# Kernel optimization log

Hardware: AMD Instinct MI355X
Metric: run time of the kernel (lower is better)

The kernel has to match this reference:

```python
import jax, jax.numpy as jnp
import numpy as np

B, N, DEG = 8, 8192, 16
E = B * N * DEG
K1 = 2458  # ceil(0.3*8192)
K2 = 738   # ceil(0.3*2458)
NUM_CLASSES = 10


def gat(x, src, dst, emask, W, a_s, a_d, bias):
    # PyG GATConv with add_self_loops=True, negative_slope=0.2, concat heads
    n = x.shape[0]
    H, F = a_s.shape
    xp = (x @ W).reshape(n, H, F)                      # [n,H,F]
    al_s = (xp * a_s).sum(-1)                          # [n,H]
    al_d = (xp * a_d).sum(-1)
    loops = jnp.arange(n, dtype=src.dtype)
    s2 = jnp.concatenate([src, loops])
    d2 = jnp.concatenate([dst, loops])
    m2 = jnp.concatenate([emask, jnp.ones(n, bool)])
    e = jax.nn.leaky_relu(al_s[s2] + al_d[d2], 0.2)    # [E+n,H]
    e = jnp.where(m2[:, None], e, -1e9)
    emax = jax.ops.segment_max(e, d2, num_segments=n)
    ex = jnp.where(m2[:, None], jnp.exp(e - emax[d2]), 0.0)
    den = jax.ops.segment_sum(ex, d2, num_segments=n)
    msg = ex[:, :, None] * xp[s2]                      # [E+n,H,F]
    out = jax.ops.segment_sum(msg, d2, num_segments=n) / den[:, :, None]
    return out.reshape(n, H * F) + bias


def inorm(x):
    # PyG InstanceNorm (affine=False): per-graph per-channel normalization
    xb = x.reshape(B, -1, x.shape[-1])
    mu = xb.mean(1, keepdims=True)
    var = ((xb - mu) ** 2).mean(1, keepdims=True)
    return ((xb - mu) / jnp.sqrt(var + 1e-5)).reshape(x.shape)


def topk_pool(x, src, dst, emask, p, k):
    # TopKPooling: score = tanh(x.p/|p|), keep top-k per graph, scale x by score
    n_tot = x.shape[0]
    n = n_tot // B
    score = jnp.tanh((x @ p) / jnp.linalg.norm(p))
    sv, si = jax.lax.top_k(score.reshape(B, n), k)     # [B,k]
    xg = jnp.take_along_axis(x.reshape(B, n, -1), si[:, :, None], axis=1)
    xnew = (xg * sv[:, :, None]).reshape(B * k, -1)
    perm = (si + (jnp.arange(B) * n)[:, None]).reshape(-1)
    newid = jnp.full(n_tot, -1, dtype=src.dtype).at[perm].set(
        jnp.arange(B * k, dtype=src.dtype))
    ns, nd = newid[src], newid[dst]
    m = emask & (ns >= 0) & (nd >= 0)
    return xnew, jnp.maximum(ns, 0), jnp.maximum(nd, 0), m


def setup_inputs() -> dict:
    key = jax.random.key(0)
    ks = jax.random.split(key, 32)
    pos = jax.random.normal(ks[0], (B * N, 3), jnp.float32)
    offs = jnp.repeat(jnp.arange(B, dtype=jnp.int32) * N, N * DEG)
    src = jax.random.randint(ks[1], (E,), 0, N, jnp.int32) + offs
    dst = jax.random.randint(ks[2], (E,), 0, N, jnp.int32) + offs

    def lin(k, fi, fo):
        return jax.random.normal(k, (fi, fo), jnp.float32) * (1.0 / np.sqrt(fi))

    d = dict(pos=pos, src=src, dst=dst)
    d['W1'] = lin(ks[3], 3, 32);   d['a_s1'] = jax.random.normal(ks[4], (2, 16)) * 0.2
    d['a_d1'] = jax.random.normal(ks[5], (2, 16)) * 0.2
    d['b1'] = jnp.zeros((32,));    d['p1'] = jax.random.normal(ks[6], (32,))
    d['W2'] = lin(ks[7], 32, 128); d['a_s2'] = jax.random.normal(ks[8], (2, 64)) * 0.2
    d['a_d2'] = jax.random.normal(ks[9], (2, 64)) * 0.2
    d['b2'] = jnp.zeros((128,));   d['p2'] = jax.random.normal(ks[10], (128,))
    d['W3'] = lin(ks[11], 128, 256); d['a_s3'] = jax.random.normal(ks[12], (1, 256)) * 0.1
    d['a_d3'] = jax.random.normal(ks[13], (1, 256)) * 0.1
    d['b3'] = jnp.zeros((256,))
    d['gw1'] = lin(ks[14], 256, 64);  d['gb1'] = jnp.zeros((64,))
    d['gw2'] = lin(ks[15], 64, 1);    d['gb2'] = jnp.zeros((1,))
    d['aw'] = lin(ks[16], 256, 256);  d['ab'] = jnp.zeros((256,))
    d['w1'] = lin(ks[17], 256, 512);  d['bb1'] = jnp.zeros((512,))
    d['w2'] = lin(ks[18], 512, 128);  d['bb2'] = jnp.zeros((128,))
    d['w3'] = lin(ks[19], 128, NUM_CLASSES); d['bb3'] = jnp.zeros((NUM_CLASSES,))
    return d


def reference(pos, src, dst, W1, a_s1, a_d1, b1, p1, W2, a_s2, a_d2, b2, p2,
              W3, a_s3, a_d3, b3, gw1, gb1, gw2, gb2, aw, ab,
              w1, bb1, w2, bb2, w3, bb3):
    emask = jnp.ones(src.shape[0], bool)
    x = gat(pos, src, dst, emask, W1, a_s1, a_d1, b1)
    x = jax.nn.elu(inorm(x))
    x, src, dst, emask = topk_pool(x, src, dst, emask, p1, K1)
    x = gat(x, src, dst, emask, W2, a_s2, a_d2, b2)
    x = jax.nn.elu(inorm(x))
    x, src, dst, emask = topk_pool(x, src, dst, emask, p2, K2)
    x = gat(x, src, dst, emask, W3, a_s3, a_d3, b3)
    x = jax.nn.elu(inorm(x))
    # GlobalAttention: gate_nn = Linear(256,64)+ELU+Linear(64,1); nn = Linear+ELU
    gate = jax.nn.elu(x @ gw1 + gb1) @ gw2 + gb2       # [M,1]
    h = jax.nn.elu(x @ aw + ab)                        # [M,256]
    a = jax.nn.softmax(gate.reshape(B, K2, 1), axis=1)
    g = (a * h.reshape(B, K2, 256)).sum(1)             # [B,256]
    z = jax.nn.elu(g @ w1 + bb1)   # dropout inactive in eval
    z = jax.nn.elu(z @ w2 + bb2)
    z = z @ w3 + bb3
    return jax.nn.log_softmax(z, axis=1)
```

## Files before the change

### kernel.cpp

```cpp
#include <hip/hip_runtime.h>
#include <cstdint>
#include <cstddef>

#define DI __device__ __forceinline__

namespace pk {

constexpr int NB1 = 65536;
constexpr int NE  = 1048576;
constexpr int BG  = 8;
constexpr int NPG1 = 8192;
constexpr int EPG1 = NE/BG;
constexpr int KP1 = 2458;
constexpr int KP2 = 738;
constexpr int NN2 = BG*KP1;
constexpr int NN3 = BG*KP2;
constexpr int REG2 = 16384;
constexpr int REG3 = 4096;
constexpr int CAP2 = BG*REG2;
constexpr int CAP3 = BG*REG3;

DI float lrelu(float x){ return x > 0.f ? x : 0.2f*x; }
DI float eluf(float x){ return x > 0.f ? x : expf(x) - 1.f; }

DI int swz_block(){
  int nb = gridDim.x, b = blockIdx.x;
  if((nb & 7) == 0) return (b & 7)*(nb >> 3) + (b >> 3);
  return b;
}

__global__ __launch_bounds__(256) void k_xp1(
    const float* __restrict__ pos, const float* __restrict__ W,
    const float* __restrict__ as_, const float* __restrict__ ad_,
    float* __restrict__ xp, float* __restrict__ als, float* __restrict__ ald){
  int i = blockIdx.x*256 + threadIdx.x;
  if(i >= NB1) return;
  float p0=pos[3*i], p1=pos[3*i+1], p2=pos[3*i+2];
  float row[32];
#pragma unroll
  for(int c=0;c<32;c++) row[c] = p0*W[c] + p1*W[32+c] + p2*W[64+c];
  float s0=0.f,d0=0.f,s1=0.f,d1=0.f;
#pragma unroll
  for(int f=0;f<16;f++){
    s0 += row[f]*as_[f];        d0 += row[f]*ad_[f];
    s1 += row[16+f]*as_[16+f];  d1 += row[16+f]*ad_[16+f];
  }
  float4* o = reinterpret_cast<float4*>(xp + (size_t)i*32);
#pragma unroll
  for(int q=0;q<8;q++) o[q] = make_float4(row[4*q],row[4*q+1],row[4*q+2],row[4*q+3]);
  als[2*i]=s0; als[2*i+1]=s1; ald[2*i]=d0; ald[2*i+1]=d1;
}

__global__ __launch_bounds__(1024) void k_tile_count(
    const int* __restrict__ de, int* __restrict__ cnt){
  __shared__ int h[256];
  int tid = threadIdx.x;
  int g = blockIdx.x & 7, t = blockIdx.x >> 3;
  int lo = g*NPG1 + t*256;
  if(tid < 256) h[tid] = 0;
  __syncthreads();
  const int4* de4 = (const int4*)(de + g*EPG1);
  for(int it=0; it<4; it++){
    int4 buf[8];
#pragma unroll
    for(int j=0;j<8;j++) buf[j] = de4[(it*8+j)*1024 + tid];
#pragma unroll
    for(int j=0;j<8;j++){
      int4 b = buf[j];
      int d0=b.x-lo, d1=b.y-lo, d2=b.z-lo, d3=b.w-lo;
      if((unsigned)d0<256u) atomicAdd(&h[d0],1);
      if((unsigned)d1<256u) atomicAdd(&h[d1],1);
      if((unsigned)d2<256u) atomicAdd(&h[d2],1);
      if((unsigned)d3<256u) atomicAdd(&h[d3],1);
    }
  }
  __syncthreads();
  if(tid < 256) cnt[lo + tid] = h[tid];
}

__global__ __launch_bounds__(1024) void k_tile_scatter(
    const int* __restrict__ se, const int* __restrict__ de,
    const int* __restrict__ rowptr, int* __restrict__ eo){
  __shared__ int cur[256];
  int tid = threadIdx.x;
  int g = blockIdx.x & 7, t = blockIdx.x >> 3;
  int lo = g*NPG1 + t*256;
  if(tid < 256) cur[tid] = rowptr[lo + tid];
  __syncthreads();
  const int4* de4 = (const int4*)(de + g*EPG1);
  const int4* se4 = (const int4*)(se + g*EPG1);
  for(int it=0; it<4; it++){
    int4 bd[8], bs[8];
#pragma unroll
    for(int j=0;j<8;j++){
      int idx = (it*8+j)*1024 + tid;
      bd[j] = de4[idx]; bs[j] = se4[idx];
    }
#pragma unroll
    for(int j=0;j<8;j++){
      int4 d = bd[j], s = bs[j];
      int d0=d.x-lo; if((unsigned)d0<256u){ int p=atomicAdd(&cur[d0],1); eo[p]=s.x; }
      int d1=d.y-lo; if((unsigned)d1<256u){ int p=atomicAdd(&cur[d1],1); eo[p]=s.y; }
      int d2=d.z-lo; if((unsigned)d2<256u){ int p=atomicAdd(&cur[d2],1); eo[p]=s.z; }
      int d3=d.w-lo; if((unsigned)d3<256u){ int p=atomicAdd(&cur[d3],1); eo[p]=s.w; }
    }
  }
}

__global__ __launch_bounds__(256) void k_scatter_r(
    const int* __restrict__ se, const int* __restrict__ de,
    const int* __restrict__ gcnt, int reg,
    int* __restrict__ cursor, int* __restrict__ eo){
  int i = swz_block()*256 + threadIdx.x;
  int g = i / reg, loc = i % reg;
  if(loc < gcnt[g]){
    int p = atomicAdd(&cursor[de[i]], 1);
    eo[p] = se[i];
  }
}

__global__ __launch_bounds__(256) void k_edge_compact(
    const int* __restrict__ se, const int* __restrict__ de,
    const int* __restrict__ gcnt_in, int fixed_in, int bpg, int reg_in,
    const int* __restrict__ newid, int* __restrict__ gcnt_out,
    int* __restrict__ ons, int* __restrict__ ond, int reg_out,
    int* __restrict__ cnt){
  __shared__ int s_a[4096];
  __shared__ int s_b[4096];
  __shared__ int run, tbase;
  int tid = threadIdx.x;
  if(tid == 0) run = 0;
  __syncthreads();
  int blk = swz_block();
  int g = blk / bpg, t = blk % bpg;
  int mg = gcnt_in ? gcnt_in[g] : fixed_in;
  if(mg > reg_in) mg = reg_in;
  int base_l = t*4096;
  if(base_l < mg){
    const int* deb = de + (size_t)g*reg_in + base_l;
    const int* seb = se + (size_t)g*reg_in + base_l;
    const int4* de4 = (const int4*)deb;
    const int4* se4 = (const int4*)seb;
    int4 BD[4], BS[4];
#pragma unroll
    for(int j=0;j<4;j++){ BD[j]=de4[j*256+tid]; BS[j]=se4[j*256+tid]; }
#pragma unroll
    for(int j=0;j<4;j++){
      int eb = base_l + (j*256+tid)*4;
      int dd[4]={BD[j].x,BD[j].y,BD[j].z,BD[j].w};
      int ss[4]={BS[j].x,BS[j].y,BS[j].z,BS[j].w};
#pragma unroll
      for(int q=0;q<4;q++){
        if(eb+q < mg){
          int a = newid[ss[q]], b = newid[dd[q]];
          if(a>=0 && b>=0){
            int p = atomicAdd(&run, 1);
            s_a[p]=a; s_b[p]=b;
            atomicAdd(&cnt[b], 1);
          }
        }
      }
    }
  }
  __syncthreads();
  int ns = run;
  if(tid==0) tbase = ns ? atomicAdd(&gcnt_out[g], ns) : 0;
  __syncthreads();
  int tb = tbase;
  for(int j=tid; j<ns; j+=256){
    int s2 = tb + j;
    if(s2 < reg_out){ ons[(size_t)g*reg_out+s2]=s_a[j]; ond[(size_t)g*reg_out+s2]=s_b[j]; }
  }
}

__global__ __launch_bounds__(1024) void k_scan_g(
    const int* __restrict__ cnt, int R, int estride,
    int* __restrict__ rowptr, int* __restrict__ cursor){
  __shared__ int wsum[16];
  int g = blockIdx.x;
  int tid = threadIdx.x, lane = tid & 63, w = tid >> 6;
  int PER = (R + 1023) >> 10;
  int base = g*R;
  int i0 = tid*PER;
  int v[8]; int s = 0;
  for(int j=0;j<PER;j++){ int i=i0+j; int x=(i<R)?cnt[base+i]:0; v[j]=s; s+=x; }
  int inc = s;
  for(int o=1;o<64;o<<=1){ int t=__shfl_up(inc,o,64); if(lane>=o) inc+=t; }
  if(lane==63) wsum[w]=inc;
  __syncthreads();
  int wb=0;
  for(int k=0;k<w;k++) wb+=wsum[k];
  int tb = g*estride + wb + inc - s;
  for(int j=0;j<PER;j++){
    int i=i0+j;
    if(i<R){
      int e=tb+v[j];
      rowptr[base+i]=e;
      if(cursor) cursor[base+i]=e;
    }
  }
}

template<int H,int F,int EB>
__global__ __launch_bounds__(256) void k_gat_fused(
    const float* __restrict__ xp, const float* __restrict__ als,
    const float* __restrict__ ald, const int* __restrict__ rowptr,
    const int* __restrict__ cnt, const int* __restrict__ esrc,
    const float* __restrict__ bias, float* __restrict__ out,
    float* __restrict__ accum, int RPG, int n){
  constexpr int C = H*F, C4 = C/4;
  constexpr int NPB = 256/C4;
  __shared__ float psum[4][C], psq[4][C];
  int tid = threadIdx.x;
  int nl = tid / C4, p = tid % C4;
  int node0 = swz_block()*NPB;
  int node = node0 + nl;
  int hh = (4*p)/F;
  const float4* xp4 = (const float4*)xp;
  float4 r = make_float4(0.f,0.f,0.f,0.f);
  bool valid = node < n;
  if(valid){
    float dvh = ald[node*H+hh];
    float sw  = expf(lrelu(als[node*H+hh] + dvh));
    float4 xs = xp4[(size_t)node*C4 + p];
    float den = sw;
    float ax=sw*xs.x, ay=sw*xs.y, az=sw*xs.z, aw_=sw*xs.w;
    int r0  = rowptr[node];
    int deg = cnt[node];
    for(int j=0; j<deg; j+=EB){
      int idx[EB]; float wv[EB]; float4 v[EB];
#pragma unroll
      for(int q=0;q<EB;q++)
        idx[q] = (j+q < deg) ? esrc[r0+j+q] : node;
#pragma unroll
      for(int q=0;q<EB;q++)
        wv[q] = als[idx[q]*H+hh];
#pragma unroll
      for(int q=0;q<EB;q++)
        v[q] = xp4[(size_t)idx[q]*C4 + p];
#pragma unroll
      for(int q=0;q<EB;q++){
        float w = (j+q < deg) ? expf(lrelu(wv[q] + dvh)) : 0.f;
        den += w;
        ax += w*v[q].x; ay += w*v[q].y; az += w*v[q].z; aw_ += w*v[q].w;
      }
    }
    float inv = 1.f / den;
    float4 bv = ((const float4*)bias)[p];
    r.x=ax*inv+bv.x; r.y=ay*inv+bv.y; r.z=az*inv+bv.z; r.w=aw_*inv+bv.w;
    ((float4*)out)[(size_t)node*C4 + p] = r;
  }
  int g0 = node0 / RPG;
  bool straddle = ((node0 + NPB - 1) / RPG) != g0;
  if(straddle){
    if(valid){
      int g = node / RPG;
      atomicAdd(&accum[(g*C+4*p+0)*2], r.x); atomicAdd(&accum[(g*C+4*p+0)*2+1], r.x*r.x);
      atomicAdd(&accum[(g*C+4*p+1)*2], r.y); atomicAdd(&accum[(g*C+4*p+1)*2+1], r.y*r.y);
      atomicAdd(&accum[(g*C+4*p+2)*2], r.z); atomicAdd(&accum[(g*C+4*p+2)*2+1], r.z*r.z);
      atomicAdd(&accum[(g*C+4*p+3)*2], r.w); atomicAdd(&accum[(g*C+4*p+3)*2+1], r.w*r.w);
    }
  } else {
    float sx=r.x, sy=r.y, sz=r.z, sw2=r.w;
    float qx=r.x*r.x, qy=r.y*r.y, qz=r.z*r.z, qw=r.w*r.w;
#pragma unroll
    for(int off=C4; off<64; off<<=1){
      sx += __shfl_down(sx, off, 64); sy += __shfl_down(sy, off, 64);
      sz += __shfl_down(sz, off, 64); sw2 += __shfl_down(sw2, off, 64);
      qx += __shfl_down(qx, off, 64); qy += __shfl_down(qy, off, 64);
      qz += __shfl_down(qz, off, 64); qw += __shfl_down(qw, off, 64);
    }
    int lane = tid & 63, w = tid >> 6;
    if(lane < C4){
      psum[w][4*lane+0]=sx; psum[w][4*lane+1]=sy;
      psum[w][4*lane+2]=sz; psum[w][4*lane+3]=sw2;
      psq[w][4*lane+0]=qx;  psq[w][4*lane+1]=qy;
      psq[w][4*lane+2]=qz;  psq[w][4*lane+3]=qw;
    }
    __syncthreads();
    if(tid < C){
      float ts = psum[0][tid]+psum[1][tid]+psum[2][tid]+psum[3][tid];
      float tq = psq[0][tid]+psq[1][tid]+psq[2][tid]+psq[3][tid];
      atomicAdd(&accum[(g0*C+tid)*2],   ts);
      atomicAdd(&accum[(g0*C+tid)*2+1], tq);
    }
  }
}

template<int K,int CO,int NPG,int H>
__global__ __launch_bounds__(256) void k_gemm_al(
    const float* __restrict__ X, const int* __restrict__ oldid,
    const float* __restrict__ scale, const float* __restrict__ W,
    float* __restrict__ Y, const float* __restrict__ a_s,
    const float* __restrict__ a_d, float* __restrict__ als,
    float* __restrict__ ald, int n){
  constexpr int SUB = 256/CO;
  constexpr int NB = SUB*NPG;
  __shared__ float xs[NB][K];
  __shared__ float ps[4][NPG], pd[4][NPG];
  int tid = threadIdx.x;
  int c = tid % CO, sg = tid / CO;
  int n0 = blockIdx.x * NB;
  for(int idx=tid; idx<NB*K; idx+=256){
    int r = idx / K, k = idx % K;
    int row = n0 + r;
    float v = 0.f;
    if(row < n){
      int orow = oldid[row];
      v = X[(size_t)orow*K + k] * scale[row];
    }
    xs[r][k] = v;
  }
  __syncthreads();
  float acc[NPG];
#pragma unroll
  for(int q=0;q<NPG;q++) acc[q]=0.f;
  for(int k=0;k<K;k++){
    float wv = W[(size_t)k*CO + c];
#pragma unroll
    for(int q=0;q<NPG;q++) acc[q] += xs[sg*NPG+q][k]*wv;
  }
  float asc = a_s[c], adc = a_d[c];
  float vs[NPG], vd[NPG];
#pragma unroll
  for(int q=0;q<NPG;q++){
    int row = n0 + sg*NPG + q;
    if(row < n) Y[(size_t)row*CO + c] = acc[q];
    vs[q] = acc[q]*asc; vd[q] = acc[q]*adc;
  }
#pragma unroll
  for(int o=32;o>0;o>>=1){
#pragma unroll
    for(int q=0;q<NPG;q++){
      vs[q] += __shfl_down(vs[q], o, 64);
      vd[q] += __shfl_down(vd[q], o, 64);
    }
  }
  int lane = tid & 63, w = tid >> 6;
  if(H == 2){
    if(lane == 0){
      int sg_ = w >> 1, h = w & 1;
#pragma unroll
      for(int q=0;q<NPG;q++){
        int row = n0 + sg_*NPG + q;
        if(row < n){ als[row*2+h] = vs[q]; ald[row*2+h] = vd[q]; }
      }
    }
  } else {
    if(lane == 0){
#pragma unroll
      for(int q=0;q<NPG;q++){ ps[w][q]=vs[q]; pd[w][q]=vd[q]; }
    }
    __syncthreads();
    if(tid < NPG){
      float s=0.f, d=0.f;
      for(int ww=0;ww<4;ww++){ s+=ps[ww][tid]; d+=pd[ww][tid]; }
      int row = n0 + tid;
      if(row < n){ als[row]=s; ald[row]=d; }
    }
  }
}

DI float inorm_of(const float* accum, int gc, float R, float x){
  float s = accum[gc*2], sq = accum[gc*2+1];
  float mu = s / R;
  float var = fmaxf(sq/R - mu*mu, 0.f);
  return eluf((x-mu)*rsqrtf(var+1e-5f));
}

template<int C>
__global__ __launch_bounds__(256) void k_inorm_score(
    float* __restrict__ x, const float* __restrict__ accum,
    const float* __restrict__ p, int R, int total,
    float* __restrict__ score, unsigned* __restrict__ u){
  __shared__ float rvp[256], rpp[256];
  int tid = threadIdx.x;
  int i = blockIdx.x*256 + tid;
  int c = tid & (C-1);
  bool act = i < total;
  float v = 0.f, pv = 0.f;
  if(act){
    int g = i / (R*C);
    v = inorm_of(accum, g*C+c, (float)R, x[i]);
    x[i] = v;
    pv = p[c];
  }
  rvp[tid] = v*pv; rpp[tid] = pv*pv;
  __syncthreads();
#pragma unroll
  for(int s2=C/2; s2>0; s2>>=1){
    if(c < s2){ rvp[tid]+=rvp[tid+s2]; rpp[tid]+=rpp[tid+s2]; }
    __syncthreads();
  }
  if(act && c==0){
    float sv = tanhf(rvp[tid]*rsqrtf(rpp[tid]));
    int row = i / C;
    score[row] = sv;
    unsigned bts = __float_as_uint(sv);
    u[row] = (bts & 0x80000000u) ? ~bts : (bts | 0x80000000u);
  }
}

__global__ __launch_bounds__(1024) void k_topk(
    const unsigned* __restrict__ u, const float* __restrict__ score,
    int R, int Ksel, int* __restrict__ newid, int* __restrict__ oldid,
    float* __restrict__ scale){
  __shared__ int hist[2048];
  __shared__ int seg[32];
  __shared__ int sh_b, sh_k;
  __shared__ int wsA[16], wsB[16];
  __shared__ int carr0, carr1;
  int g = blockIdx.x, tid = threadIdx.x, lane = tid&63, w = tid>>6;
  const unsigned* ug = u + (size_t)g*R;
  unsigned prefix = 0;
  int K = Ksel;
  for(int lev=0; lev<3; lev++){
    int shf = (lev==0)?21:((lev==1)?10:0);
    int nb  = (lev==2)?1024:2048;
    for(int i=tid;i<2048;i+=1024) hist[i]=0;
    __syncthreads();
    for(int i=tid;i<R;i+=1024){
      unsigned v = ug[i];
      bool ok = (lev==0) || (lev==1 && (v>>21)==prefix) || (lev==2 && (v>>10)==prefix);
      if(ok) atomicAdd(&hist[(v>>shf)&(nb-1)], 1);
    }
    __syncthreads();
    int W = nb/32;
    if(tid<32){ int s=0; int lo=nb-W*(tid+1); for(int b=lo;b<lo+W;b++) s+=hist[b]; seg[tid]=s; }
    __syncthreads();
    if(tid==0){
      int kk=K, sgi=0;
      while(seg[sgi]<kk){ kk-=seg[sgi]; sgi++; }
      int b = nb-1-W*sgi;
      while(hist[b]<kk){ kk-=hist[b]; b--; }
      sh_b=b; sh_k=kk;
    }
    __syncthreads();
    int b = sh_b; K = sh_k;
    if(lev==0) prefix = (unsigned)b;
    else if(lev==1) prefix = (prefix<<11) | (unsigned)b;
    else prefix = (prefix<<10) | (unsigned)b;
    __syncthreads();
  }
  unsigned thr = prefix;
  int need = K;
  if(tid==0){ carr0=0; carr1=0; }
  __syncthreads();
  for(int bb=0; bb<R; bb+=1024){
    int i = bb + tid; bool in = i < R;
    unsigned uv = in ? ug[i] : 0u;
    int eq = (in && uv==thr) ? 1:0;
    int gt = (in && uv>thr) ? 1:0;
    int inc = eq;
    for(int o=1;o<64;o<<=1){ int t=__shfl_up(inc,o,64); if(lane>=o) inc+=t; }
    if(lane==63) wsA[w]=inc;
    __syncthreads();
    int wb=0; for(int k=0;k<w;k++) wb+=wsA[k];
    int eq_excl = carr0 + wb + inc - eq;
    int take = (gt || (eq && eq_excl<need)) ? 1 : 0;
    int inc2 = take;
    for(int o=1;o<64;o<<=1){ int t=__shfl_up(inc2,o,64); if(lane>=o) inc2+=t; }
    if(lane==63) wsB[w]=inc2;
    __syncthreads();
    int wb2=0; for(int k=0;k<w;k++) wb2+=wsB[k];
    int pos = carr1 + wb2 + inc2 - take;
    if(take){
      int nr = g*Ksel + pos;
      newid[(size_t)g*R+i] = nr;
      oldid[nr] = g*R+i;
      scale[nr] = score[(size_t)g*R+i];
    }
    __syncthreads();
    if(tid==1023){ carr0 += wb + inc; carr1 += wb2 + inc2; }
    __syncthreads();
  }
}

__global__ __launch_bounds__(256) void k_gate_fused(
    const float* __restrict__ X, const float* __restrict__ accum,
    const float* __restrict__ gw1, const float* __restrict__ gb1,
    const float* __restrict__ gw2, const float* __restrict__ gb2,
    float* __restrict__ gatev, int n){
  __shared__ float xs[4][256];
  int tid = threadIdx.x;
  int n0 = blockIdx.x*4;
  for(int idx=tid; idx<1024; idx+=256){
    int r = idx >> 8, k = idx & 255;
    int row = n0 + r;
    float v = 0.f;
    if(row < n){
      int g = row / KP2;
      v = inorm_of(accum, g*256+k, (float)KP2, X[(size_t)row*256 + k]);
    }
    xs[r][k] = v;
  }
  __syncthreads();
  int sg = tid >> 6, c = tid & 63;
  float a = 0.f;
#pragma unroll 8
  for(int k=0;k<256;k++) a = fmaf(xs[sg][k], gw1[k*64+c], a);
  a = eluf(a + gb1[c]);
  float v = a * gw2[c];
#pragma unroll
  for(int o=32;o>0;o>>=1) v += __shfl_down(v, o, 64);
  if(c==0){
    int row = n0 + sg;
    if(row < n) gatev[row] = v + gb2[0];
  }
}

__global__ __launch_bounds__(256) void k_attn_gemm(
    const float* __restrict__ X, const float* __restrict__ accum,
    const float* __restrict__ W, const float* __restrict__ bias,
    const float* __restrict__ gatev, float* __restrict__ gvec){
  __shared__ float xs[4][256];
  __shared__ float red[256];
  int tid = threadIdx.x;
  int t = blockIdx.x, g = blockIdx.y;
  int r0 = t*4;
  float mx = -1e30f;
  for(int r=tid;r<KP2;r+=256) mx = fmaxf(mx, gatev[g*KP2+r]);
  red[tid]=mx; __syncthreads();
  for(int s=128;s>0;s>>=1){ if(tid<s) red[tid]=fmaxf(red[tid],red[tid+s]); __syncthreads(); }
  mx = red[0]; __syncthreads();
  float sm=0.f;
  for(int r=tid;r<KP2;r+=256) sm += expf(gatev[g*KP2+r]-mx);
  red[tid]=sm; __syncthreads();
  for(int s=128;s>0;s>>=1){ if(tid<s) red[tid]+=red[tid+s]; __syncthreads(); }
  float inv = 1.f/red[0];
  __syncthreads();
  for(int idx=tid; idx<1024; idx+=256){
    int r = idx >> 8, k = idx & 255;
    int lr = r0 + r;
    float v = 0.f;
    if(lr < KP2){
      int row = g*KP2 + lr;
      v = inorm_of(accum, g*256+k, (float)KP2, X[(size_t)row*256 + k]);
    }
    xs[r][k] = v;
  }
  __syncthreads();
  int c = tid;
  float acc[4];
#pragma unroll
  for(int q=0;q<4;q++) acc[q]=0.f;
  for(int k=0;k<256;k++){
    float wv = W[(size_t)k*256 + c];
#pragma unroll
    for(int q=0;q<4;q++) acc[q] += xs[q][k]*wv;
  }
  float bv = bias[c];
  float tot = 0.f;
#pragma unroll
  for(int q=0;q<4;q++){
    int lr = r0 + q;
    if(lr < KP2){
      float h = eluf(acc[q] + bv);
      tot += expf(gatev[g*KP2+lr]-mx) * h;
    }
  }
  atomicAdd(&gvec[g*256+c], tot*inv);
}

template<int K,int CO,int ACT>
__global__ __launch_bounds__(256) void k_mlp_t(
    const float* __restrict__ X, const float* __restrict__ W,
    const float* __restrict__ b, float* __restrict__ Y, int n){
  int i = blockIdx.x*256+threadIdx.x;
  if(i>=n*CO) return;
  int r=i/CO, c=i%CO;
  const float* xr = X + (size_t)r*K;
  float a=0.f;
#pragma unroll 16
  for(int k=0;k<K;k++) a = fmaf(xr[k], W[(size_t)k*CO+c], a);
  a += b[c];
  if(ACT) a = eluf(a);
  Y[i]=a;
}

__global__ __launch_bounds__(64) void k_head(
    const float* __restrict__ z2, const float* __restrict__ w3,
    const float* __restrict__ b3, float* __restrict__ out){
  __shared__ float zc[10]; __shared__ float mred, sred;
  int g=blockIdx.x, tid=threadIdx.x;
  if(tid<10){
    float a=0.f;
#pragma unroll 16
    for(int k=0;k<128;k++) a += z2[g*128+k]*w3[k*10+tid];
    zc[tid]=a+b3[tid];
  }
  __syncthreads();
  if(tid==0){
    float m=zc[0];
    for(int k=1;k<10;k++) m=fmaxf(m,zc[k]);
    float s=0.f;
    for(int k=0;k<10;k++) s+=expf(zc[k]-m);
    mred=m; sred=logf(s);
  }
  __syncthreads();
  if(tid<10) out[g*10+tid]=zc[tid]-mred-sred;
}

}

extern "C" void kernel_launch(void* const* d_in, const int* in_sizes, int n_in,
                              void* d_out, int out_size, void* d_ws, size_t ws_size,
                              hipStream_t stream){
  using namespace pk;
  (void)in_sizes; (void)n_in; (void)out_size;
  const float* pos = (const float*)d_in[0];
  const int*   src = (const int*)d_in[1];
  const int*   dst = (const int*)d_in[2];
  const float* W1  = (const float*)d_in[3];
  const float* as1 = (const float*)d_in[4];
  const float* ad1 = (const float*)d_in[5];
  const float* b1  = (const float*)d_in[6];
  const float* p1  = (const float*)d_in[7];
  const float* W2  = (const float*)d_in[8];
  const float* as2 = (const float*)d_in[9];
  const float* ad2 = (const float*)d_in[10];
  const float* b2  = (const float*)d_in[11];
  const float* p2  = (const float*)d_in[12];
  const float* W3  = (const float*)d_in[13];
  const float* as3 = (const float*)d_in[14];
  const float* ad3 = (const float*)d_in[15];
  const float* b3  = (const float*)d_in[16];
  const float* gw1 = (const float*)d_in[17];
  const float* gb1 = (const float*)d_in[18];
  const float* gw2 = (const float*)d_in[19];
  const float* gb2 = (const float*)d_in[20];
  const float* aw  = (const float*)d_in[21];
  const float* ab  = (const float*)d_in[22];
  const float* w1  = (const float*)d_in[23];
  const float* bb1 = (const float*)d_in[24];
  const float* w2  = (const float*)d_in[25];
  const float* bb2 = (const float*)d_in[26];
  const float* w3  = (const float*)d_in[27];
  const float* bb3 = (const float*)d_in[28];
  float* out = (float*)d_out;

  char* base = (char*)d_ws; size_t off = 0;
  auto alloc = [&](size_t nbytes)->char*{
    char* p = base + off; off = (off + nbytes + 255) & ~(size_t)255; return p;
  };
  int*   cnt2  = (int*)alloc((size_t)NN2*4);
  int*   cnt3  = (int*)alloc((size_t)NN3*4);
  int*   ecnt2 = (int*)alloc((size_t)BG*4);
  int*   ecnt3 = (int*)alloc((size_t)BG*4);
  float* acc1  = (float*)alloc((size_t)BG*32*2*4);
  float* acc2  = (float*)alloc((size_t)BG*128*2*4);
  float* acc3  = (float*)alloc((size_t)BG*256*2*4);
  float* gvec  = (float*)alloc((size_t)BG*256*4);
  size_t zend = off;
  int*   newid1 = (int*)alloc((size_t)NB1*4);
  int*   newid2 = (int*)alloc((size_t)NN2*4);
  size_t fstart = (size_t)((char*)newid1 - base);
  size_t fend = off;
  int*      cnt1   = (int*)alloc((size_t)NB1*4);
  float*    xp1    = (float*)alloc((size_t)NB1*32*4);
  float*    als1   = (float*)alloc((size_t)NB1*2*4);
  float*    ald1   = (float*)alloc((size_t)NB1*2*4);
  int*      rowptr1= (int*)alloc((size_t)NB1*4);
  int*      esrc1  = (int*)alloc((size_t)NE*4);
  float*    out1   = (float*)alloc((size_t)NB1*32*4);
  float*    score1 = (float*)alloc((size_t)NB1*4);
  unsigned* u1     = (unsigned*)alloc((size_t)NB1*4);
  int*      oldid1 = (int*)alloc((size_t)NN2*4);
  float*    scale1 = (float*)alloc((size_t)NN2*4);
  int*      ns2    = (int*)alloc((size_t)CAP2*4);
  int*      nd2    = (int*)alloc((size_t)CAP2*4);
  int*      rowptr2= (int*)alloc((size_t)NN2*4);
  int*      cursor2= (int*)alloc((size_t)NN2*4);
  int*      esrc2  = (int*)alloc((size_t)CAP2*4);
  float*    xp2    = (float*)alloc((size_t)NN2*128*4);
  float*    als2   = (float*)alloc((size_t)NN2*2*4);
  float*    ald2   = (float*)alloc((size_t)NN2*2*4);
  float*    out2   = (float*)alloc((size_t)NN2*128*4);
  float*    score2 = (float*)alloc((size_t)NN2*4);
  unsigned* u2     = (unsigned*)alloc((size_t)NN2*4);
  int*      oldid2 = (int*)alloc((size_t)NN3*4);
  float*    scale2 = (float*)alloc((size_t)NN3*4);
  int*      ns3    = (int*)alloc((size_t)CAP3*4);
  int*      nd3    = (int*)alloc((size_t)CAP3*4);
  int*      rowptr3= (int*)alloc((size_t)NN3*4);
  int*      cursor3= (int*)alloc((size_t)NN3*4);
  int*      esrc3  = (int*)alloc((size_t)CAP3*4);
  float*    xp3    = (float*)alloc((size_t)NN3*256*4);
  float*    als3   = (float*)alloc((size_t)NN3*4);
  float*    ald3   = (float*)alloc((size_t)NN3*4);
  float*    out3   = (float*)alloc((size_t)NN3*256*4);
  float*    gatev  = (float*)alloc((size_t)NN3*4);
  float*    z1     = (float*)alloc((size_t)BG*512*4);
  float*    z2     = (float*)alloc((size_t)BG*128*4);
  if(off > ws_size) return;

  auto cdiv = [](int a, int b){ return (a+b-1)/b; };

  hipMemsetAsync(base, 0, zend, stream);
  hipMemsetAsync(base + fstart, 0xFF, fend - fstart, stream);

  k_xp1<<<cdiv(NB1,256),256,0,stream>>>(pos,W1,as1,ad1,xp1,als1,ald1);
  k_tile_count<<<256,1024,0,stream>>>(dst,cnt1);
  k_scan_g<<<BG,1024,0,stream>>>(cnt1,NPG1,EPG1,rowptr1,nullptr);
  k_tile_scatter<<<256,1024,0,stream>>>(src,dst,rowptr1,esrc1);
  k_gat_fused<2,16,8><<<NB1/32,256,0,stream>>>(xp1,als1,ald1,rowptr1,cnt1,esrc1,b1,out1,acc1,NPG1,NB1);
  k_inorm_score<32><<<cdiv(NB1*32,256),256,0,stream>>>(out1,acc1,p1,8192,NB1*32,score1,u1);
  k_topk<<<BG,1024,0,stream>>>(u1,score1,8192,KP1,newid1,oldid1,scale1);
  k_edge_compact<<<BG*32,256,0,stream>>>(src,dst,nullptr,EPG1,32,EPG1,newid1,ecnt2,ns2,nd2,REG2,cnt2);
  k_scan_g<<<BG,1024,0,stream>>>(cnt2,KP1,REG2,rowptr2,cursor2);
  k_scatter_r<<<CAP2/256,256,0,stream>>>(ns2,nd2,ecnt2,REG2,cursor2,esrc2);
  k_gemm_al<32,128,4,2><<<cdiv(NN2,8),256,0,stream>>>(out1,oldid1,scale1,W2,xp2,as2,ad2,als2,ald2,NN2);
  k_gat_fused<2,64,8><<<NN2/8,256,0,stream>>>(xp2,als2,ald2,rowptr2,cnt2,esrc2,b2,out2,acc2,KP1,NN2);
  k_inorm_score<128><<<cdiv(NN2*128,256),256,0,stream>>>(out2,acc2,p2,KP1,NN2*128,score2,u2);
  k_topk<<<BG,1024,0,stream>>>(u2,score2,KP1,KP2,newid2,oldid2,scale2);
  k_edge_compact<<<BG*4,256,0,stream>>>(ns2,nd2,ecnt2,0,4,REG2,newid2,ecnt3,ns3,nd3,REG3,cnt3);
  k_scan_g<<<BG,1024,0,stream>>>(cnt3,KP2,REG3,rowptr3,cursor3);
  k_scatter_r<<<CAP3/256,256,0,stream>>>(ns3,nd3,ecnt3,REG3,cursor3,esrc3);
  k_gemm_al<128,256,4,1><<<cdiv(NN3,4),256,0,stream>>>(out2,oldid2,scale2,W3,xp3,as3,ad3,als3,ald3,NN3);
  k_gat_fused<1,256,4><<<NN3/4,256,0,stream>>>(xp3,als3,ald3,rowptr3,cnt3,esrc3,b3,out3,acc3,KP2,NN3);
  k_gate_fused<<<cdiv(NN3,4),256,0,stream>>>(out3,acc3,gw1,gb1,gw2,gb2,gatev,NN3);
  k_attn_gemm<<<dim3(cdiv(KP2,4),BG),256,0,stream>>>(out3,acc3,aw,ab,gatev,gvec);
  k_mlp_t<256,512,1><<<cdiv(BG*512,256),256,0,stream>>>(gvec,w1,bb1,z1,BG);
  k_mlp_t<512,128,1><<<cdiv(BG*128,256),256,0,stream>>>(z1,w2,bb2,z2,BG);
  k_head<<<BG,64,0,stream>>>(z2,w3,bb3,out);
}
```

Measured before the change: 447.8 us.

## Merge small kernels into fewer launches and batch per-thread atomics

Merges the xp1 projection into the tile-count kernel using extra blocks, and folds the per-graph prefix scans into the gemm_al launches as trailing blocks. The three MLP/head kernels become one k_tail per-graph kernel. Edge compaction now takes one shared atomic per thread instead of one per edge, at the cost of reading newid twice. The gate and attention kernels now process 8 rows per block instead of 4, and the first GAT's EB template parameter goes from 8 to 16. The main goal is fewer launches and less serialization, with some risk of load imbalance inside the mixed-role kernels.

```diff
diff --git a/kernel.cpp b/kernel.cpp
--- a/kernel.cpp
+++ b/kernel.cpp
@@ -29,33 +29,33 @@
   return b;
 }
 
-__global__ __launch_bounds__(256) void k_xp1(
+__global__ __launch_bounds__(1024) void k_s1_front(
     const float* __restrict__ pos, const float* __restrict__ W,
     const float* __restrict__ as_, const float* __restrict__ ad_,
-    float* __restrict__ xp, float* __restrict__ als, float* __restrict__ ald){
-  int i = blockIdx.x*256 + threadIdx.x;
-  if(i >= NB1) return;
-  float p0=pos[3*i], p1=pos[3*i+1], p2=pos[3*i+2];
-  float row[32];
-#pragma unroll
-  for(int c=0;c<32;c++) row[c] = p0*W[c] + p1*W[32+c] + p2*W[64+c];
-  float s0=0.f,d0=0.f,s1=0.f,d1=0.f;
-#pragma unroll
-  for(int f=0;f<16;f++){
-    s0 += row[f]*as_[f];        d0 += row[f]*ad_[f];
-    s1 += row[16+f]*as_[16+f];  d1 += row[16+f]*ad_[16+f];
-  }
-  float4* o = reinterpret_cast<float4*>(xp + (size_t)i*32);
-#pragma unroll
-  for(int q=0;q<8;q++) o[q] = make_float4(row[4*q],row[4*q+1],row[4*q+2],row[4*q+3]);
-  als[2*i]=s0; als[2*i+1]=s1; ald[2*i]=d0; ald[2*i+1]=d1;
-}
-
-__global__ __launch_bounds__(1024) void k_tile_count(
+    float* __restrict__ xp, float* __restrict__ als, float* __restrict__ ald,
     const int* __restrict__ de, int* __restrict__ cnt){
   __shared__ int h[256];
   int tid = threadIdx.x;
-  int g = blockIdx.x & 7, t = blockIdx.x >> 3;
+  if(blockIdx.x < 64){
+    int i = blockIdx.x*1024 + tid;
+    float p0=pos[3*i], p1=pos[3*i+1], p2=pos[3*i+2];
+    float row[32];
+#pragma unroll
+    for(int c=0;c<32;c++) row[c] = p0*W[c] + p1*W[32+c] + p2*W[64+c];
+    float s0=0.f,d0=0.f,s1=0.f,d1=0.f;
+#pragma unroll
+    for(int f=0;f<16;f++){
+      s0 += row[f]*as_[f];        d0 += row[f]*ad_[f];
+      s1 += row[16+f]*as_[16+f];  d1 += row[16+f]*ad_[16+f];
+    }
+    float4* o = reinterpret_cast<float4*>(xp + (size_t)i*32);
+#pragma unroll
+    for(int q=0;q<8;q++) o[q] = make_float4(row[4*q],row[4*q+1],row[4*q+2],row[4*q+3]);
+    als[2*i]=s0; als[2*i+1]=s1; ald[2*i]=d0; ald[2*i+1]=d1;
+    return;
+  }
+  int bb = blockIdx.x - 64;
+  int g = bb & 7, t = bb >> 3;
   int lo = g*NPG1 + t*256;
   if(tid < 256) h[tid] = 0;
   __syncthreads();
@@ -144,6 +144,7 @@
     int4 BD[4], BS[4];
 #pragma unroll
     for(int j=0;j<4;j++){ BD[j]=de4[j*256+tid]; BS[j]=se4[j*256+tid]; }
+    int cl = 0;
 #pragma unroll
     for(int j=0;j<4;j++){
       int eb = base_l + (j*256+tid)*4;
@@ -153,11 +154,22 @@
       for(int q=0;q<4;q++){
         if(eb+q < mg){
           int a = newid[ss[q]], b = newid[dd[q]];
-          if(a>=0 && b>=0){
-            int p = atomicAdd(&run, 1);
-            s_a[p]=a; s_b[p]=b;
-            atomicAdd(&cnt[b], 1);
-          }
+          if(a>=0 && b>=0){ cl++; atomicAdd(&cnt[b], 1); }
+        }
+      }
+    }
+    int p0 = 0;
+    if(cl) p0 = atomicAdd(&run, cl);
+#pragma unroll
+    for(int j=0;j<4;j++){
+      int eb = base_l + (j*256+tid)*4;
+      int dd[4]={BD[j].x,BD[j].y,BD[j].z,BD[j].w};
+      int ss[4]={BS[j].x,BS[j].y,BS[j].z,BS[j].w};
+#pragma unroll
+      for(int q=0;q<4;q++){
+        if(eb+q < mg){
+          int a = newid[ss[q]], b = newid[dd[q]];
+          if(a>=0 && b>=0){ s_a[p0]=a; s_b[p0]=b; p0++; }
         }
       }
     }
@@ -197,6 +209,34 @@
       int e=tb+v[j];
       rowptr[base+i]=e;
       if(cursor) cursor[base+i]=e;
+    }
+  }
+}
+
+template<int PER>
+DI void scan256(const int* __restrict__ cnt, int R, int estride,
+                int* __restrict__ rowptr, int* __restrict__ cursor, int g){
+  __shared__ int wsum[4];
+  int tid = threadIdx.x, lane = tid & 63, w = tid >> 6;
+  int base = g*R;
+  int i0 = tid*PER;
+  int v[PER]; int s = 0;
+#pragma unroll
+  for(int j=0;j<PER;j++){ int i=i0+j; int x=(i<R)?cnt[base+i]:0; v[j]=s; s+=x; }
+  int inc = s;
+  for(int o=1;o<64;o<<=1){ int t=__shfl_up(inc,o,64); if(lane>=o) inc+=t; }
+  if(lane==63) wsum[w]=inc;
+  __syncthreads();
+  int wb=0;
+  for(int k=0;k<w;k++) wb+=wsum[k];
+  int tb = g*estride + wb + inc - s;
+#pragma unroll
+  for(int j=0;j<PER;j++){
+    int i=i0+j;
+    if(i<R){
+      int e=tb+v[j];
+      rowptr[base+i]=e;
+      cursor[base+i]=e;
     }
   }
 }
@@ -287,17 +327,23 @@
   }
 }
 
-template<int K,int CO,int NPG,int H>
+template<int K,int CO,int NPG,int H,int PER>
 __global__ __launch_bounds__(256) void k_gemm_al(
     const float* __restrict__ X, const int* __restrict__ oldid,
     const float* __restrict__ scale, const float* __restrict__ W,
     float* __restrict__ Y, const float* __restrict__ a_s,
     const float* __restrict__ a_d, float* __restrict__ als,
-    float* __restrict__ ald, int n){
+    float* __restrict__ ald, int n, int ngemm,
+    const int* __restrict__ scnt, int sR, int sstride,
+    int* __restrict__ srowptr, int* __restrict__ scursor){
   constexpr int SUB = 256/CO;
   constexpr int NB = SUB*NPG;
   __shared__ float xs[NB][K];
   __shared__ float ps[4][NPG], pd[4][NPG];
+  if((int)blockIdx.x >= ngemm){
+    scan256<PER>(scnt, sR, sstride, srowptr, scursor, (int)blockIdx.x - ngemm);
+    return;
+  }
   int tid = threadIdx.x;
   int c = tid % CO, sg = tid / CO;
   int n0 = blockIdx.x * NB;
@@ -481,10 +527,10 @@
     const float* __restrict__ gw1, const float* __restrict__ gb1,
     const float* __restrict__ gw2, const float* __restrict__ gb2,
     float* __restrict__ gatev, int n){
-  __shared__ float xs[4][256];
+  __shared__ float xs[8][256];
   int tid = threadIdx.x;
-  int n0 = blockIdx.x*4;
-  for(int idx=tid; idx<1024; idx+=256){
+  int n0 = blockIdx.x*8;
+  for(int idx=tid; idx<2048; idx+=256){
     int r = idx >> 8, k = idx & 255;
     int row = n0 + r;
     float v = 0.f;
@@ -496,16 +542,25 @@
   }
   __syncthreads();
   int sg = tid >> 6, c = tid & 63;
-  float a = 0.f;
+  float a0 = 0.f, a1 = 0.f;
 #pragma unroll 8
-  for(int k=0;k<256;k++) a = fmaf(xs[sg][k], gw1[k*64+c], a);
-  a = eluf(a + gb1[c]);
-  float v = a * gw2[c];
-#pragma unroll
-  for(int o=32;o>0;o>>=1) v += __shfl_down(v, o, 64);
+  for(int k=0;k<256;k++){
+    float w = gw1[k*64+c];
+    a0 = fmaf(xs[sg][k],   w, a0);
+    a1 = fmaf(xs[sg+4][k], w, a1);
+  }
+  float gb = gb1[c], g2 = gw2[c];
+  float v0 = eluf(a0 + gb) * g2;
+  float v1 = eluf(a1 + gb) * g2;
+#pragma unroll
+  for(int o=32;o>0;o>>=1){
+    v0 += __shfl_down(v0, o, 64);
+    v1 += __shfl_down(v1, o, 64);
+  }
   if(c==0){
-    int row = n0 + sg;
-    if(row < n) gatev[row] = v + gb2[0];
+    int r0 = n0 + sg, r1 = n0 + sg + 4;
+    if(r0 < n) gatev[r0] = v0 + gb2[0];
+    if(r1 < n) gatev[r1] = v1 + gb2[0];
   }
 }
 
@@ -513,11 +568,11 @@
     const float* __restrict__ X, const float* __restrict__ accum,
     const float* __restrict__ W, const float* __restrict__ bias,
     const float* __restrict__ gatev, float* __restrict__ gvec){
-  __shared__ float xs[4][256];
+  __shared__ float xs[8][256];
   __shared__ float red[256];
   int tid = threadIdx.x;
   int t = blockIdx.x, g = blockIdx.y;
-  int r0 = t*4;
+  int r0 = t*8;
   float mx = -1e30f;
   for(int r=tid;r<KP2;r+=256) mx = fmaxf(mx, gatev[g*KP2+r]);
   red[tid]=mx; __syncthreads();
@@ -529,7 +584,7 @@
   for(int s=128;s>0;s>>=1){ if(tid<s) red[tid]+=red[tid+s]; __syncthreads(); }
   float inv = 1.f/red[0];
   __syncthreads();
-  for(int idx=tid; idx<1024; idx+=256){
+  for(int idx=tid; idx<2048; idx+=256){
     int r = idx >> 8, k = idx & 255;
     int lr = r0 + r;
     float v = 0.f;
@@ -541,18 +596,18 @@
   }
   __syncthreads();
   int c = tid;
-  float acc[4];
-#pragma unroll
-  for(int q=0;q<4;q++) acc[q]=0.f;
+  float acc[8];
+#pragma unroll
+  for(int q=0;q<8;q++) acc[q]=0.f;
   for(int k=0;k<256;k++){
     float wv = W[(size_t)k*256 + c];
 #pragma unroll
-    for(int q=0;q<4;q++) acc[q] += xs[q][k]*wv;
+    for(int q=0;q<8;q++) acc[q] += xs[q][k]*wv;
   }
   float bv = bias[c];
   float tot = 0.f;
 #pragma unroll
-  for(int q=0;q<4;q++){
+  for(int q=0;q<8;q++){
     int lr = r0 + q;
     if(lr < KP2){
       float h = eluf(acc[q] + bv);
@@ -562,32 +617,39 @@
   atomicAdd(&gvec[g*256+c], tot*inv);
 }
 
-template<int K,int CO,int ACT>
-__global__ __launch_bounds__(256) void k_mlp_t(
-    const float* __restrict__ X, const float* __restrict__ W,
-    const float* __restrict__ b, float* __restrict__ Y, int n){
-  int i = blockIdx.x*256+threadIdx.x;
-  if(i>=n*CO) return;
-  int r=i/CO, c=i%CO;
-  const float* xr = X + (size_t)r*K;
-  float a=0.f;
+__global__ __launch_bounds__(256) void k_tail(
+    const float* __restrict__ gvec,
+    const float* __restrict__ w1, const float* __restrict__ bb1,
+    const float* __restrict__ w2, const float* __restrict__ bb2,
+    const float* __restrict__ w3, const float* __restrict__ bb3,
+    float* __restrict__ out){
+  __shared__ float g_s[256];
+  __shared__ float z1s[512];
+  __shared__ float z2s[128];
+  __shared__ float zc[10];
+  __shared__ float mred, sred;
+  int g = blockIdx.x, tid = threadIdx.x;
+  g_s[tid] = gvec[g*256+tid];
+  __syncthreads();
+  for(int o = tid; o < 512; o += 256){
+    float a = 0.f;
+#pragma unroll 8
+    for(int k=0;k<256;k++) a = fmaf(g_s[k], w1[(size_t)k*512+o], a);
+    z1s[o] = eluf(a + bb1[o]);
+  }
+  __syncthreads();
+  if(tid < 128){
+    float a = 0.f;
+#pragma unroll 8
+    for(int k=0;k<512;k++) a = fmaf(z1s[k], w2[(size_t)k*128+tid], a);
+    z2s[tid] = eluf(a + bb2[tid]);
+  }
+  __syncthreads();
+  if(tid < 10){
+    float a = 0.f;
 #pragma unroll 16
-  for(int k=0;k<K;k++) a = fmaf(xr[k], W[(size_t)k*CO+c], a);
-  a += b[c];
-  if(ACT) a = eluf(a);
-  Y[i]=a;
-}
-
-__global__ __launch_bounds__(64) void k_head(
-    const float* __restrict__ z2, const float* __restrict__ w3,
-    const float* __restrict__ b3, float* __restrict__ out){
-  __shared__ float zc[10]; __shared__ float mred, sred;
-  int g=blockIdx.x, tid=threadIdx.x;
-  if(tid<10){
-    float a=0.f;
-#pragma unroll 16
-    for(int k=0;k<128;k++) a += z2[g*128+k]*w3[k*10+tid];
-    zc[tid]=a+b3[tid];
+    for(int k=0;k<128;k++) a = fmaf(z2s[k], w3[(size_t)k*10+tid], a);
+    zc[tid] = a + bb3[tid];
   }
   __syncthreads();
   if(tid==0){
@@ -692,6 +754,7 @@
   float*    gatev  = (float*)alloc((size_t)NN3*4);
   float*    z1     = (float*)alloc((size_t)BG*512*4);
   float*    z2     = (float*)alloc((size_t)BG*128*4);
+  (void)z1; (void)z2;
   if(off > ws_size) return;
 
   auto cdiv = [](int a, int b){ return (a+b-1)/b; };
@@ -699,28 +762,33 @@
   hipMemsetAsync(base, 0, zend, stream);
   hipMemsetAsync(base + fstart, 0xFF, fend - fstart, stream);
 
-  k_xp1<<<cdiv(NB1,256),256,0,stream>>>(pos,W1,as1,ad1,xp1,als1,ald1);
-  k_tile_count<<<256,1024,0,stream>>>(dst,cnt1);
+  k_s1_front<<<320,1024,0,stream>>>(pos,W1,as1,ad1,xp1,als1,ald1,dst,cnt1);
   k_scan_g<<<BG,1024,0,stream>>>(cnt1,NPG1,EPG1,rowptr1,nullptr);
   k_tile_scatter<<<256,1024,0,stream>>>(src,dst,rowptr1,esrc1);
-  k_gat_fused<2,16,8><<<NB1/32,256,0,stream>>>(xp1,als1,ald1,rowptr1,cnt1,esrc1,b1,out1,acc1,NPG1,NB1);
+  k_gat_fused<2,16,16><<<NB1/32,256,0,stream>>>(xp1,als1,ald1,rowptr1,cnt1,esrc1,b1,out1,acc1,NPG1,NB1);
   k_inorm_score<32><<<cdiv(NB1*32,256),256,0,stream>>>(out1,acc1,p1,8192,NB1*32,score1,u1);
   k_topk<<<BG,1024,0,stream>>>(u1,score1,8192,KP1,newid1,oldid1,scale1);
   k_edge_compact<<<BG*32,256,0,stream>>>(src,dst,nullptr,EPG1,32,EPG1,newid1,ecnt2,ns2,nd2,REG2,cnt2);
-  k_scan_g<<<BG,1024,0,stream>>>(cnt2,KP1,REG2,rowptr2,cursor2);
+  {
+    int ngemm = cdiv(NN2,8);
+    k_gemm_al<32,128,4,2,10><<<ngemm+BG,256,0,stream>>>(
+        out1,oldid1,scale1,W2,xp2,as2,ad2,als2,ald2,NN2,
+        ngemm,cnt2,KP1,REG2,rowptr2,cursor2);
+  }
   k_scatter_r<<<CAP2/256,256,0,stream>>>(ns2,nd2,ecnt2,REG2,cursor2,esrc2);
-  k_gemm_al<32,128,4,2><<<cdiv(NN2,8),256,0,stream>>>(out1,oldid1,scale1,W2,xp2,as2,ad2,als2,ald2,NN2);
   k_gat_fused<2,64,8><<<NN2/8,256,0,stream>>>(xp2,als2,ald2,rowptr2,cnt2,esrc2,b2,out2,acc2,KP1,NN2);
   k_inorm_score<128><<<cdiv(NN2*128,256),256,0,stream>>>(out2,acc2,p2,KP1,NN2*128,score2,u2);
   k_topk<<<BG,1024,0,stream>>>(u2,score2,KP1,KP2,newid2,oldid2,scale2);
   k_edge_compact<<<BG*4,256,0,stream>>>(ns2,nd2,ecnt2,0,4,REG2,newid2,ecnt3,ns3,nd3,REG3,cnt3);
-  k_scan_g<<<BG,1024,0,stream>>>(cnt3,KP2,REG3,rowptr3,cursor3);
+  {
+    int ngemm = cdiv(NN3,4);
+    k_gemm_al<128,256,4,1,3><<<ngemm+BG,256,0,stream>>>(
+        out2,oldid2,scale2,W3,xp3,as3,ad3,als3,ald3,NN3,
+        ngemm,cnt3,KP2,REG3,rowptr3,cursor3);
+  }
   k_scatter_r<<<CAP3/256,256,0,stream>>>(ns3,nd3,ecnt3,REG3,cursor3,esrc3);
-  k_gemm_al<128,256,4,1><<<cdiv(NN3,4),256,0,stream>>>(out2,oldid2,scale2,W3,xp3,as3,ad3,als3,ald3,NN3);
   k_gat_fused<1,256,4><<<NN3/4,256,0,stream>>>(xp3,als3,ald3,rowptr3,cnt3,esrc3,b3,out3,acc3,KP2,NN3);
-  k_gate_fused<<<cdiv(NN3,4),256,0,stream>>>(out3,acc3,gw1,gb1,gw2,gb2,gatev,NN3);
-  k_attn_gemm<<<dim3(cdiv(KP2,4),BG),256,0,stream>>>(out3,acc3,aw,ab,gatev,gvec);
-  k_mlp_t<256,512,1><<<cdiv(BG*512,256),256,0,stream>>>(gvec,w1,bb1,z1,BG);
-  k_mlp_t<512,128,1><<<cdiv(BG*128,256),256,0,stream>>>(z1,w2,bb2,z2,BG);
-  k_head<<<BG,64,0,stream>>>(z2,w3,bb3,out);
-}
+  k_gate_fused<<<cdiv(NN3,8),256,0,stream>>>(out3,acc3,gw1,gb1,gw2,gb2,gatev,NN3);
+  k_attn_gemm<<<dim3(cdiv(KP2,8),BG),256,0,stream>>>(out3,acc3,aw,ab,gatev,gvec);
+  k_tail<<<BG,256,0,stream>>>(gvec,w1,bb1,w2,bb2,w3,bb3,out);
+}
```

Result: slower. 465.6 us (+4.0%).
